# Kernel optimization log

Measured on AMD Instinct MI355X. Metric: run time of the kernel, lower is better.

Reference implementation:

```python
import jax, jax.numpy as jnp
import numpy as np
import math

NH, NKV, D = 32, 8, 128  # heads, kv heads, head dim

def _alibi_slopes(n):
    cp2 = 2 ** math.floor(math.log2(n))
    base = 2.0 ** (-8.0 / cp2)
    slopes = base ** np.arange(1, cp2 + 1, dtype=np.float32)
    if cp2 != n:
        extra_base = 2.0 ** (-4.0 / cp2)
        extra = extra_base ** np.arange(1, 1 + 2 * (n - cp2), 2, dtype=np.float32)
        slopes = np.concatenate([slopes, extra])
    return slopes.astype(np.float32)

def setup_inputs() -> dict:
    key = jax.random.key(0)
    k1, k2, k3 = jax.random.split(key, 3)
    B, S, H = 4, 1024, 4096
    qkv_out = NH * D + 2 * NKV * D  # 6144
    return {
        "hidden_states": jax.random.normal(k1, (B, S, H), jnp.float32) * 0.02,
        "w_qkv": jax.random.normal(k2, (H, qkv_out), jnp.float32) * 0.02,
        "w_o": jax.random.normal(k3, (NH * D, H), jnp.float32) * 0.02,
    }

def reference(hidden_states, w_qkv, w_o):
    B, S, H = hidden_states.shape
    G = NH // NKV  # query groups per kv head
    scale = D ** -0.5

    qkv = hidden_states @ w_qkv  # [B,S,6144]
    q = qkv[..., : NH * D].reshape(B, S, NKV, G, D)
    k = qkv[..., NH * D : NH * D + NKV * D].reshape(B, S, NKV, D)
    v = qkv[..., NH * D + NKV * D :].reshape(B, S, NKV, D)

    scores = jnp.einsum("bqhgd,bkhd->bhgqk", q, k) * scale  # [B,NKV,G,S,S]

    slopes = jnp.asarray(_alibi_slopes(NH)).reshape(NKV, G)  # head order
    pos = jnp.arange(S)
    rel = pos[:, None] - pos[None, :]  # i - j
    sqrt_dist = jnp.sqrt(jnp.maximum(rel, 0).astype(jnp.float32))
    bias = -slopes[:, :, None, None] * sqrt_dist  # ALiBi-sqrt bias
    bias = jnp.where(rel[None, None] >= 0, bias, -jnp.inf)  # causal mask

    attn = jax.nn.softmax(scores + bias[None], axis=-1)
    out = jnp.einsum("bhgqk,bkhd->bqhgd", attn, v).reshape(B, S, NH * D)
    return out @ w_o
```

## Files before the change

kernel.cpp:

```cpp
#include <hip/hip_runtime.h>
#include <stdint.h>

typedef __attribute__((ext_vector_type(4))) float floatx4;
typedef __attribute__((ext_vector_type(8))) short short8;
typedef unsigned short ushort_t;

#define DEVI __device__ __forceinline__

constexpr int Bc   = 4;
constexpr int Sc   = 1024;
constexpr int Hc   = 4096;
constexpr int NHc  = 32;
constexpr int NKVc = 8;
constexpr int Dc   = 128;
constexpr int QKVO = 6144;
constexpr int Mc   = Bc * Sc;

DEVI ushort_t f2bf(float f) {
  union { float f; unsigned u; } x; x.f = f;
  unsigned u = x.u;
  u += 0x7fffu + ((u >> 16) & 1u);
  return (ushort_t)(u >> 16);
}

DEVI short8 cvt8(floatx4 a, floatx4 b) {
  short8 r;
  r[0] = (short)f2bf(a[0]); r[1] = (short)f2bf(a[1]);
  r[2] = (short)f2bf(a[2]); r[3] = (short)f2bf(a[3]);
  r[4] = (short)f2bf(b[0]); r[5] = (short)f2bf(b[1]);
  r[6] = (short)f2bf(b[2]); r[7] = (short)f2bf(b[3]);
  return r;
}

DEVI void load_lds16(const ushort_t* g, ushort_t* l) {
  __builtin_amdgcn_global_load_lds(
      (const __attribute__((address_space(1))) void*)g,
      (__attribute__((address_space(3))) void*)l, 16, 0, 0);
}

#define BARRIER()  asm volatile("s_barrier" ::: "memory")
#define LGKM0()    asm volatile("s_waitcnt lgkmcnt(0)" ::: "memory")
#define VMCNT(n)   asm volatile("s_waitcnt vmcnt(" #n ")" ::: "memory")

__global__ __launch_bounds__(256)
void cvt_bf16(const float* __restrict__ src, ushort_t* __restrict__ dst, int n8)
{
  const int i = blockIdx.x * 256 + threadIdx.x;
  if (i >= n8) return;
  const floatx4 f0 = *(const floatx4*)(src + (size_t)i * 8);
  const floatx4 f1 = *(const floatx4*)(src + (size_t)i * 8 + 4);
  *(short8*)(dst + (size_t)i * 8) = cvt8(f0, f1);
}

__global__ __launch_bounds__(256)
void transpose_cvt(const float* __restrict__ src, ushort_t* __restrict__ dst,
                   int R, int C)
{
  __shared__ float ts[64][67];
  const int cb = C >> 6;
  const int r0 = (blockIdx.x / cb) << 6;
  const int c0 = (blockIdx.x % cb) << 6;
  const int t  = threadIdx.x;

  const int lr = t >> 4, lc = (t & 15) << 2;
#pragma unroll
  for (int i = 0; i < 4; ++i) {
    const floatx4 v = *(const floatx4*)(src + (size_t)(r0 + lr + 16 * i) * C + c0 + lc);
#pragma unroll
    for (int j = 0; j < 4; ++j) ts[lr + 16 * i][lc + j] = v[j];
  }
  __syncthreads();

  const int c     = ((t >> 6) << 4) + ((t & 63) >> 2);
  const int chunk = t & 3;
  short8 t0, t1;
#pragma unroll
  for (int k = 0; k < 8; ++k) t0[k] = (short)f2bf(ts[chunk * 16 + k][c]);
#pragma unroll
  for (int k = 0; k < 8; ++k) t1[k] = (short)f2bf(ts[chunk * 16 + 8 + k][c]);
  ushort_t* dp = dst + (size_t)(c0 + c) * R + r0 + chunk * 16;
  *(short8*)dp       = t0;
  *(short8*)(dp + 8) = t1;
}

__global__ __launch_bounds__(256)
void v_transpose(const ushort_t* __restrict__ qkv, ushort_t* __restrict__ vt)
{
  __shared__ ushort_t ts[64][72];
  const int bid = blockIdx.x;
  const int db  = bid & 1;
  const int sb  = (bid >> 1) & 15;
  const int hkv = (bid >> 5) & 7;
  const int b   = bid >> 8;
  const int t   = threadIdx.x;

  const ushort_t* src = qkv + (size_t)(b * Sc + sb * 64) * QKVO
                        + (NHc * Dc + NKVc * Dc) + hkv * Dc + db * 64;
  const int lr = t >> 3, lc = (t & 7) * 8;
  *(short8*)&ts[lr][lc]      = *(const short8*)(src + (size_t)lr * QKVO + lc);
  *(short8*)&ts[lr + 32][lc] = *(const short8*)(src + (size_t)(lr + 32) * QKVO + lc);
  __syncthreads();

  ushort_t* dst = vt + ((size_t)(b * NKVc + hkv) * Dc + db * 64) * Sc + sb * 64;
  const int dr  = t >> 2;
  const int sc0 = (t & 3) * 16;
  short8 o0, o1;
#pragma unroll
  for (int k = 0; k < 8; ++k) o0[k] = (short)ts[sc0 + k][dr];
#pragma unroll
  for (int k = 0; k < 8; ++k) o1[k] = (short)ts[sc0 + 8 + k][dr];
  *(short8*)(dst + (size_t)dr * Sc + sc0)     = o0;
  *(short8*)(dst + (size_t)dr * Sc + sc0 + 8) = o1;
}

template<int NFRAG, bool OBF16>
__global__ __launch_bounds__(512, 2)
void gemm_nt8d(const ushort_t* __restrict__ A, const ushort_t* __restrict__ BT,
               void* __restrict__ Cp, int M, int N, int K)
{
  constexpr int BN = 64 * NFRAG;
  __shared__ __align__(16) ushort_t As[2][256 * 64];
  __shared__ __align__(16) ushort_t Bs[2][BN * 64];

  const int nb  = N / BN;
  const int nwg = (M >> 8) * nb;
  int bid = blockIdx.x;
  bid = (bid & 7) * (nwg >> 3) + (bid >> 3);
  const int bm = bid / nb, bn = bid % nb;
  const int m0 = bm << 8, n0 = bn * BN;

  const int tid  = threadIdx.x;
  const int wid  = tid >> 6, lane = tid & 63;
  const int wm   = wid >> 2, wn = wid & 3;
  const int fr   = lane & 15;
  const int g16  = (lane >> 4) << 4;
  const int rsw  = (fr & 7) << 4;
  const int l8   = lane >> 3;
  const int scol = ((lane & 7) ^ l8) << 3;

  const int sr   = (wid << 3);
  const size_t Ks = (size_t)K;
  const ushort_t* agS = A  + (size_t)(m0 + sr + l8) * K + scol;
  const ushort_t* bgS = BT + (size_t)(n0 + sr + l8) * K + scol;

  const int rowA = (wm * 128 + fr) * 128;
  const int rowB = (wn * 16 * NFRAG + fr) * 128;
  const int cb0  = g16 ^ rsw;
  const int cb1  = (64 + g16) ^ rsw;

  const floatx4 fz = {0.f, 0.f, 0.f, 0.f};
  floatx4 acc[8][NFRAG];
#pragma unroll
  for (int i = 0; i < 8; ++i)
#pragma unroll
    for (int f = 0; f < NFRAG; ++f) acc[i][f] = fz;

  auto SAq0 = [&](int s, size_t kn) {
    load_lds16(agS + kn,            &As[s][(sr +   0) * 64]);
    load_lds16(agS + 128 * Ks + kn, &As[s][(sr + 128) * 64]);
  };
  auto SAq1 = [&](int s, size_t kn) {
    load_lds16(agS +  64 * Ks + kn, &As[s][(sr +  64) * 64]);
    load_lds16(agS + 192 * Ks + kn, &As[s][(sr + 192) * 64]);
  };
  auto SB01 = [&](int s, size_t kn) {
    load_lds16(bgS + kn,            &Bs[s][(sr +   0) * 64]);
    load_lds16(bgS +  64 * Ks + kn, &Bs[s][(sr +  64) * 64]);
  };
  auto SB2 = [&](int s, size_t kn) {
    load_lds16(bgS + 128 * Ks + kn, &Bs[s][(sr + 128) * 64]);
    if constexpr (NFRAG == 4)
      load_lds16(bgS + 192 * Ks + kn, &Bs[s][(sr + 192) * 64]);
  };

  SAq0(0, 0); SAq1(0, 0); SB01(0, 0); SB2(0, 0);
  SAq0(1, 64); SB01(1, 64); SB2(1, 64);
  VMCNT(0);
  BARRIER();

#define LDA(s, i, ks) (*(const short8*)((const char*)&As[s][0] + rowA + (i) * 2048 + ((ks) ? cb1 : cb0)))
#define LDB(s, f, ks) (*(const short8*)((const char*)&Bs[s][0] + rowB + (f) * 2048 + ((ks) ? cb1 : cb0)))

  const int NI = K >> 7;
  for (int it = 0; it < NI; ++it) {
    const size_t kt0 = (size_t)it << 7;
    const size_t k1 = kt0 + 64, k2 = kt0 + 128, k3 = kt0 + 192;
    const bool st2 = (it + 1 < NI);
    const bool st3 = st2;

    short8 aR[4], bR[NFRAG][2], bS[NFRAG][2];

#define MFMA_PH(base, barr, ks)                                              \
    __builtin_amdgcn_s_setprio(1);                                          \
    _Pragma("unroll")                                                       \
    for (int i = 0; i < 4; ++i)                                             \
      _Pragma("unroll")                                                     \
      for (int f = 0; f < NFRAG; ++f)                                       \
        acc[(base) + i][f] = __builtin_amdgcn_mfma_f32_16x16x32_bf16(       \
            aR[i], barr[f][ks], acc[(base) + i][f], 0, 0, 0);               \
    __builtin_amdgcn_s_setprio(0);

#pragma unroll
    for (int i = 0; i < 4; ++i) aR[i] = LDA(0, i, 0);
#pragma unroll
    for (int f = 0; f < NFRAG; ++f) { bR[f][0] = LDB(0, f, 0); bR[f][1] = LDB(0, f, 1); }
    SAq1(1, k1);
    VMCNT(4);
    BARRIER();
    LGKM0(); __builtin_amdgcn_sched_barrier(0);
    MFMA_PH(0, bR, 0)
    BARRIER();

#pragma unroll
    for (int i = 0; i < 4; ++i) aR[i] = LDA(1, i, 0);
#pragma unroll
    for (int f = 0; f < NFRAG; ++f) { bS[f][0] = LDB(1, f, 0); bS[f][1] = LDB(1, f, 1); }
    if (st2) SB01(0, k2);
    VMCNT(4);
    BARRIER();
    LGKM0(); __builtin_amdgcn_sched_barrier(0);
    MFMA_PH(0, bS, 0)
    BARRIER();

#pragma unroll
    for (int i = 0; i < 4; ++i) aR[i] = LDA(0, 4 + i, 0);
    if (st2) SB2(0, k2);
    if constexpr (NFRAG == 4) { VMCNT(4); } else { VMCNT(3); }
    BARRIER();
    LGKM0(); __builtin_amdgcn_sched_barrier(0);
    MFMA_PH(4, bR, 0)
    BARRIER();

#pragma unroll
    for (int i = 0; i < 4; ++i) aR[i] = LDA(1, 4 + i, 0);
    if (st3) SB01(1, k3);
    BARRIER();
    LGKM0(); __builtin_amdgcn_sched_barrier(0);
    MFMA_PH(4, bS, 0)
    BARRIER();

#pragma unroll
    for (int i = 0; i < 4; ++i) aR[i] = LDA(0, i, 1);
    if (st3) SB2(1, k3);
    BARRIER();
    LGKM0(); __builtin_amdgcn_sched_barrier(0);
    MFMA_PH(0, bR, 1)
    BARRIER();

#pragma unroll
    for (int i = 0; i < 4; ++i) aR[i] = LDA(1, i, 1);
    if (st2) SAq0(0, k2);
    BARRIER();
    LGKM0(); __builtin_amdgcn_sched_barrier(0);
    MFMA_PH(0, bS, 1)
    BARRIER();

#pragma unroll
    for (int i = 0; i < 4; ++i) aR[i] = LDA(0, 4 + i, 1);
    if (st3) SAq0(1, k3);
    BARRIER();
    LGKM0(); __builtin_amdgcn_sched_barrier(0);
    MFMA_PH(4, bR, 1)
    BARRIER();

#pragma unroll
    for (int i = 0; i < 4; ++i) aR[i] = LDA(1, 4 + i, 1);
    if (st2) SAq1(0, k2);
    VMCNT(4);
    BARRIER();
    LGKM0(); __builtin_amdgcn_sched_barrier(0);
    MFMA_PH(4, bS, 1)
    BARRIER();

#undef MFMA_PH
  }
#undef LDA
#undef LDB

  const int r4 = (lane >> 4) << 2;
#pragma unroll
  for (int i = 0; i < 8; ++i) {
#pragma unroll
    for (int rr = 0; rr < 4; ++rr) {
      const size_t row = (size_t)(m0 + wm * 128 + i * 16 + r4 + rr);
#pragma unroll
      for (int f = 0; f < NFRAG; ++f) {
        const size_t col = (size_t)(n0 + wn * 16 * NFRAG + f * 16 + fr);
        if constexpr (OBF16)
          ((ushort_t*)Cp)[row * N + col] = f2bf(acc[i][f][rr]);
        else
          ((float*)Cp)[row * N + col] = acc[i][f][rr];
      }
    }
  }
}

__global__ __launch_bounds__(256, 2)
void attn_fwd(const ushort_t* __restrict__ qkv,
              const ushort_t* __restrict__ vt,
              ushort_t* __restrict__ attn)
{
  __shared__ __align__(16) ushort_t Plds[4][32 * 40];

  const int bid = blockIdx.x;
  const int x   = bid & 7;
  const int p   = bid >> 3;
  const int j   = p & 15;
  const int g   = ((p >> 4) << 3) + x;
  const int b   = g >> 3;
  const int hkv = g & 7;

  const int tid  = threadIdx.x;
  const int wid  = tid >> 6, lane = tid & 63;
  const int h    = hkv * 4 + wid;
  const int fr   = lane & 15;
  const int kk8  = (lane >> 4) << 3;
  const int q4   = (lane >> 4) << 2;
  const float slope = exp2f(-0.25f * (float)(h + 1));
  const float scale = 0.08838834764831845f;

  const ushort_t* qp  = qkv + (size_t)b * Sc * QKVO + (size_t)h * Dc;
  const ushort_t* kp  = qkv + (size_t)b * Sc * QKVO + NHc * Dc + (size_t)hkv * Dc;
  const ushort_t* vtp = vt + (size_t)(b * NKVc + hkv) * Dc * Sc;
  ushort_t* myP = &Plds[wid][0];

  const floatx4 fz = {0.f, 0.f, 0.f, 0.f};

  auto process = [&](const int qb) {
    short8 qf[2][4];
#pragma unroll
    for (int t = 0; t < 2; ++t) {
      const int qrow = qb * 32 + t * 16 + fr;
#pragma unroll
      for (int s = 0; s < 4; ++s)
        qf[t][s] = *(const short8*)(qp + (size_t)qrow * QKVO + s * 32 + kk8);
    }

    floatx4 o[2][8];
#pragma unroll
    for (int t = 0; t < 2; ++t)
#pragma unroll
      for (int jj = 0; jj < 8; ++jj) o[t][jj] = fz;
    float mrow[2][4], lrow[2][4];
#pragma unroll
    for (int t = 0; t < 2; ++t)
#pragma unroll
      for (int rr = 0; rr < 4; ++rr) { mrow[t][rr] = -1e30f; lrow[t][rr] = 0.f; }

    for (int kb = 0; kb <= qb; ++kb) {
      floatx4 s_[2][2];
      s_[0][0] = fz; s_[0][1] = fz; s_[1][0] = fz; s_[1][1] = fz;
#pragma unroll
      for (int half = 0; half < 2; ++half) {
        const int kcol = kb * 32 + half * 16 + fr;
#pragma unroll
        for (int s = 0; s < 4; ++s) {
          const short8 kf = *(const short8*)(kp + (size_t)kcol * QKVO + s * 32 + kk8);
          s_[0][half] = __builtin_amdgcn_mfma_f32_16x16x32_bf16(qf[0][s], kf, s_[0][half], 0, 0, 0);
          s_[1][half] = __builtin_amdgcn_mfma_f32_16x16x32_bf16(qf[1][s], kf, s_[1][half], 0, 0, 0);
        }
      }

      short8 vf[8];
#pragma unroll
      for (int jj = 0; jj < 8; ++jj)
        vf[jj] = *(const short8*)(vtp + (size_t)(jj * 16 + fr) * Sc + kb * 32 + kk8);

#pragma unroll
      for (int t = 0; t < 2; ++t)
#pragma unroll
        for (int rr = 0; rr < 4; ++rr) {
          const int qg  = qb * 32 + t * 16 + q4 + rr;
          const int dk0 = qg - (kb * 32 + fr);
          const int dk1 = dk0 - 16;
          s_[t][0][rr] = (dk0 >= 0)
              ? s_[t][0][rr] * scale - slope * sqrtf((float)dk0) : -1e30f;
          s_[t][1][rr] = (dk1 >= 0)
              ? s_[t][1][rr] * scale - slope * sqrtf((float)dk1) : -1e30f;
        }

      float pmv[2][4];
#pragma unroll
      for (int t = 0; t < 2; ++t)
#pragma unroll
        for (int rr = 0; rr < 4; ++rr) {
          float pm = fmaxf(s_[t][0][rr], s_[t][1][rr]);
#pragma unroll
          for (int m = 1; m < 16; m <<= 1) pm = fmaxf(pm, __shfl_xor(pm, m));
          pmv[t][rr] = pm;
        }

      int need = 0;
#pragma unroll
      for (int t = 0; t < 2; ++t)
#pragma unroll
        for (int rr = 0; rr < 4; ++rr)
          need |= (pmv[t][rr] > mrow[t][rr] + 8.f) ? 1 : 0;
      if (__any(need)) {
#pragma unroll
        for (int t = 0; t < 2; ++t)
#pragma unroll
          for (int rr = 0; rr < 4; ++rr) {
            const float mnew = fmaxf(mrow[t][rr], pmv[t][rr]);
            const float corr = __expf(mrow[t][rr] - mnew);
            lrow[t][rr] *= corr;
            mrow[t][rr] = mnew;
#pragma unroll
            for (int jj = 0; jj < 8; ++jj) o[t][jj][rr] *= corr;
          }
      }

#pragma unroll
      for (int t = 0; t < 2; ++t)
#pragma unroll
        for (int rr = 0; rr < 4; ++rr) {
          const float p0 = __expf(s_[t][0][rr] - mrow[t][rr]);
          const float p1 = __expf(s_[t][1][rr] - mrow[t][rr]);
          lrow[t][rr] += p0 + p1;
          myP[(t * 16 + q4 + rr) * 40 + fr]      = f2bf(p0);
          myP[(t * 16 + q4 + rr) * 40 + 16 + fr] = f2bf(p1);
        }
      short8 pa[2];
      pa[0] = *(const short8*)&myP[fr * 40 + kk8];
      pa[1] = *(const short8*)&myP[(16 + fr) * 40 + kk8];

#pragma unroll
      for (int jj = 0; jj < 8; ++jj) {
        o[0][jj] = __builtin_amdgcn_mfma_f32_16x16x32_bf16(pa[0], vf[jj], o[0][jj], 0, 0, 0);
        o[1][jj] = __builtin_amdgcn_mfma_f32_16x16x32_bf16(pa[1], vf[jj], o[1][jj], 0, 0, 0);
      }
    }

#pragma unroll
    for (int t = 0; t < 2; ++t)
#pragma unroll
      for (int rr = 0; rr < 4; ++rr) {
        float rs = lrow[t][rr];
#pragma unroll
        for (int m = 1; m < 16; m <<= 1) rs += __shfl_xor(rs, m);
        const float inv = 1.f / rs;
        const size_t tok = (size_t)b * Sc + qb * 32 + t * 16 + q4 + rr;
#pragma unroll
        for (int jj = 0; jj < 8; ++jj)
          attn[tok * (size_t)(NHc * Dc) + h * Dc + jj * 16 + fr] = f2bf(o[t][jj][rr] * inv);
      }
  };

  process(31 - j);
  process(j);
}

extern "C" void kernel_launch(void* const* d_in, const int* in_sizes, int n_in,
                              void* d_out, int out_size, void* d_ws, size_t ws_size,
                              hipStream_t stream)
{
  const float* hidden = (const float*)d_in[0];
  const float* w_qkv  = (const float*)d_in[1];
  const float* w_o    = (const float*)d_in[2];
  float* out = (float*)d_out;

  ushort_t* wqT   = (ushort_t*)d_ws;
  ushort_t* hidb  = wqT + (size_t)QKVO * Hc;
  ushort_t* qkvb  = hidb + (size_t)Mc * Hc;
  ushort_t* attnb = hidb;
  ushort_t* woT   = wqT;
  ushort_t* vtb   = wqT + (size_t)Mc * Hc;

  cvt_bf16<<<dim3((Mc * Hc / 8) / 256), dim3(256), 0, stream>>>(
      hidden, hidb, Mc * Hc / 8);
  transpose_cvt<<<dim3((Hc / 64) * (QKVO / 64)), dim3(256), 0, stream>>>(
      w_qkv, wqT, Hc, QKVO);
  gemm_nt8d<3, true><<<dim3((Mc / 256) * (QKVO / 192)), dim3(512), 0, stream>>>(
      hidb, wqT, qkvb, Mc, QKVO, Hc);
  v_transpose<<<dim3(1024), dim3(256), 0, stream>>>(qkvb, vtb);
  attn_fwd<<<dim3(512), dim3(256), 0, stream>>>(qkvb, vtb, attnb);
  transpose_cvt<<<dim3((Hc / 64) * (Hc / 64)), dim3(256), 0, stream>>>(
      w_o, woT, Hc, Hc);
  gemm_nt8d<4, false><<<dim3((Mc / 256) * (Hc / 256)), dim3(512), 0, stream>>>(
      attnb, woT, out, Mc, Hc, Hc);
}
```

Baseline: 619.8 us.

## Add double-buffered ping-pong GEMM variant for output projection

Adds a new gemm_nt8 kernel that double-buffers A and B tiles in LDS, splits each K-step into four MFMA phases, and interleaves the asynchronous global-to-LDS loads for the next tile between them with explicit vmcnt waits, barriers and setprio. The output projection GEMM is switched to this kernel. The aim is to hide global memory latency behind matrix-core work. In exchange it uses more LDS per block and adds more barriers, which may lower occupancy or add synchronisation stalls.

```diff
diff --git a/kernel.cpp b/kernel.cpp
--- a/kernel.cpp
+++ b/kernel.cpp
@@ -295,6 +295,161 @@
   }
 }
 
+template<int NFRAG, bool OBF16>
+__global__ __launch_bounds__(512, 2)
+void gemm_nt8(const ushort_t* __restrict__ A, const ushort_t* __restrict__ BT,
+              void* __restrict__ Cp, int M, int N, int K)
+{
+  constexpr int BN = 64 * NFRAG;
+  __shared__ __align__(16) ushort_t As[2][256 * 64];
+  __shared__ __align__(16) ushort_t Bs[2][BN * 64];
+
+  const int nb  = N / BN;
+  const int nwg = (M >> 8) * nb;
+  int bid = blockIdx.x;
+  bid = (bid & 7) * (nwg >> 3) + (bid >> 3);
+  const int bm = bid / nb, bn = bid % nb;
+  const int m0 = bm << 8, n0 = bn * BN;
+
+  const int tid  = threadIdx.x;
+  const int wid  = tid >> 6, lane = tid & 63;
+  const int wm   = wid >> 2, wn = wid & 3;
+  const int fr   = lane & 15;
+  const int g16  = (lane >> 4) << 4;
+  const int rsw  = (fr & 7) << 4;
+  const int l8   = lane >> 3;
+  const int scol = ((lane & 7) ^ l8) << 3;
+
+  const int sr   = (wid << 3);
+  const size_t Ks = (size_t)K;
+  const ushort_t* agS = A  + (size_t)(m0 + sr + l8) * K + scol;
+  const ushort_t* bgS = BT + (size_t)(n0 + sr + l8) * K + scol;
+
+  const int rowA = (wm * 128 + fr) * 128;
+  const int rowB = (wn * 16 * NFRAG + fr) * 128;
+  const int cb0  = g16 ^ rsw;
+  const int cb1  = (64 + g16) ^ rsw;
+
+  const floatx4 fz = {0.f, 0.f, 0.f, 0.f};
+  floatx4 acc[8][NFRAG];
+#pragma unroll
+  for (int i = 0; i < 8; ++i)
+#pragma unroll
+    for (int f = 0; f < NFRAG; ++f) acc[i][f] = fz;
+
+  auto STB = [&](int v, size_t kn) {
+#pragma unroll
+    for (int j = 0; j < NFRAG; ++j)
+      load_lds16(bgS + (size_t)(64 * j) * Ks + kn, &Bs[v][(sr + 64 * j) * 64]);
+  };
+  auto STA = [&](int v, size_t kn) {
+    load_lds16(agS + kn,            &As[v][(sr +   0) * 64]);
+    load_lds16(agS + 128 * Ks + kn, &As[v][(sr + 128) * 64]);
+    load_lds16(agS +  64 * Ks + kn, &As[v][(sr +  64) * 64]);
+    load_lds16(agS + 192 * Ks + kn, &As[v][(sr + 192) * 64]);
+  };
+
+  STB(0, 0); STA(0, 0);
+  VMCNT(2);
+  BARRIER();
+
+  const int NT = K >> 6;
+  for (int kt = 0; kt < NT; ++kt) {
+    const int u = kt & 1, v = u ^ 1;
+    const char* Au = (const char*)&As[u][0];
+    const char* Bu = (const char*)&Bs[u][0];
+    const bool st  = (kt + 1 < NT);
+    const size_t kn = (size_t)(kt + 1) << 6;
+
+#define LDA(i, ks) (*(const short8*)(Au + rowA + (i) * 2048 + ((ks) ? cb1 : cb0)))
+#define LDB(f, ks) (*(const short8*)(Bu + rowB + (f) * 2048 + ((ks) ? cb1 : cb0)))
+
+    short8 aR[4], bR[NFRAG];
+
+#pragma unroll
+    for (int i = 0; i < 4; ++i) aR[i] = LDA(i, 0);
+#pragma unroll
+    for (int f = 0; f < NFRAG; ++f) bR[f] = LDB(f, 0);
+    if (st) {
+      STB(v, kn);
+      if constexpr (NFRAG == 4) { VMCNT(4); } else { VMCNT(3); }
+    } else { VMCNT(0); }
+    BARRIER();
+    LGKM0(); __builtin_amdgcn_sched_barrier(0);
+    __builtin_amdgcn_s_setprio(1);
+#pragma unroll
+    for (int i = 0; i < 4; ++i)
+#pragma unroll
+      for (int f = 0; f < NFRAG; ++f)
+        acc[i][f] = __builtin_amdgcn_mfma_f32_16x16x32_bf16(aR[i], bR[f], acc[i][f], 0, 0, 0);
+    __builtin_amdgcn_s_setprio(0);
+    BARRIER();
+
+#pragma unroll
+    for (int i = 0; i < 4; ++i) aR[i] = LDA(4 + i, 0);
+    if (st) STA(v, kn);
+    BARRIER();
+    LGKM0(); __builtin_amdgcn_sched_barrier(0);
+    __builtin_amdgcn_s_setprio(1);
+#pragma unroll
+    for (int i = 0; i < 4; ++i)
+#pragma unroll
+      for (int f = 0; f < NFRAG; ++f)
+        acc[4 + i][f] = __builtin_amdgcn_mfma_f32_16x16x32_bf16(aR[i], bR[f], acc[4 + i][f], 0, 0, 0);
+    __builtin_amdgcn_s_setprio(0);
+    BARRIER();
+
+#pragma unroll
+    for (int i = 0; i < 4; ++i) aR[i] = LDA(4 + i, 1);
+#pragma unroll
+    for (int f = 0; f < NFRAG; ++f) bR[f] = LDB(f, 1);
+    BARRIER();
+    LGKM0(); __builtin_amdgcn_sched_barrier(0);
+    __builtin_amdgcn_s_setprio(1);
+#pragma unroll
+    for (int i = 0; i < 4; ++i)
+#pragma unroll
+      for (int f = 0; f < NFRAG; ++f)
+        acc[4 + i][f] = __builtin_amdgcn_mfma_f32_16x16x32_bf16(aR[i], bR[f], acc[4 + i][f], 0, 0, 0);
+    __builtin_amdgcn_s_setprio(0);
+    BARRIER();
+
+#pragma unroll
+    for (int i = 0; i < 4; ++i) aR[i] = LDA(i, 1);
+    if (st) { VMCNT(2); }
+    BARRIER();
+    LGKM0(); __builtin_amdgcn_sched_barrier(0);
+    __builtin_amdgcn_s_setprio(1);
+#pragma unroll
+    for (int i = 0; i < 4; ++i)
+#pragma unroll
+      for (int f = 0; f < NFRAG; ++f)
+        acc[i][f] = __builtin_amdgcn_mfma_f32_16x16x32_bf16(aR[i], bR[f], acc[i][f], 0, 0, 0);
+    __builtin_amdgcn_s_setprio(0);
+    BARRIER();
+
+#undef LDA
+#undef LDB
+  }
+
+  const int r4 = (lane >> 4) << 2;
+#pragma unroll
+  for (int i = 0; i < 8; ++i) {
+#pragma unroll
+    for (int rr = 0; rr < 4; ++rr) {
+      const size_t row = (size_t)(m0 + wm * 128 + i * 16 + r4 + rr);
+#pragma unroll
+      for (int f = 0; f < NFRAG; ++f) {
+        const size_t col = (size_t)(n0 + wn * 16 * NFRAG + f * 16 + fr);
+        if constexpr (OBF16)
+          ((ushort_t*)Cp)[row * N + col] = f2bf(acc[i][f][rr]);
+        else
+          ((float*)Cp)[row * N + col] = acc[i][f][rr];
+      }
+    }
+  }
+}
+
 __global__ __launch_bounds__(256, 2)
 void attn_fwd(const ushort_t* __restrict__ qkv,
               const ushort_t* __restrict__ vt,
@@ -476,6 +631,6 @@
   attn_fwd<<<dim3(512), dim3(256), 0, stream>>>(qkvb, vtb, attnb);
   transpose_cvt<<<dim3((Hc / 64) * (Hc / 64)), dim3(256), 0, stream>>>(
       w_o, woT, Hc, Hc);
-  gemm_nt8d<4, false><<<dim3((Mc / 256) * (Hc / 256)), dim3(512), 0, stream>>>(
+  gemm_nt8<4, false><<<dim3((Mc / 256) * (Hc / 256)), dim3(512), 0, stream>>>(
       attnb, woT, out, Mc, Hc, Hc);
 }
```

Result: faster. 561.2 us (-9.5%).
